# Optimization experiments

Hardware: AMD Instinct MI355X
Metric: run time of the kernel (lower is better)

Reference implementation:

```python
import jax, jax.numpy as jnp
import numpy as np

B, N, D, F, K = 32, 128, 3, 64, 50
EPS = 1e-6  # distances_from_vectors eps


def setup_inputs() -> dict:
    key = jax.random.key(0)
    ks = jax.random.split(key, 24)
    s = 0.1
    rn = lambda k, shape: (jax.random.normal(k, shape, jnp.float32) * s)
    return {
        "t": jnp.zeros((1,), jnp.float32),
        "xs": jax.random.normal(ks[0], (B, N * D), jnp.float32),
        "mus": jnp.linspace(0.0, 5.0, K).astype(jnp.float32),
        "gamma": jnp.array([10.0], jnp.float32),
        "W_enc": rn(ks[1], (1, F)), "b_enc": rn(ks[2], (F,)),
        "cf1_W1": rn(ks[3], (K, F)), "cf1_b1": rn(ks[4], (F,)),
        "cf1_W2": rn(ks[5], (F, F)), "cf1_b2": rn(ks[6], (F,)),
        "cf2_W1": rn(ks[7], (K, F)), "cf2_b1": rn(ks[8], (F,)),
        "cf2_W2": rn(ks[9], (F, F)), "cf2_b2": rn(ks[10], (F,)),
        "cf3_W1": rn(ks[11], (K, F)), "cf3_b1": rn(ks[12], (F,)),
        "cf3_W2": rn(ks[13], (F, F)), "cf3_b2": rn(ks[14], (F,)),
        "Wt1": rn(ks[15], (F, F)), "bt1": rn(ks[16], (F,)),
        "Wt2": rn(ks[17], (F, 1)), "bt2": rn(ks[18], (1,)),
    }


def reference(t, xs, mus, gamma, W_enc, b_enc,
              cf1_W1, cf1_b1, cf1_W2, cf1_b2,
              cf2_W1, cf2_b1, cf2_W2, cf2_b2,
              cf3_W1, cf3_b1, cf3_W2, cf3_b2,
              Wt1, bt1, Wt2, bt2):
    # off-diagonal neighbor index: row i -> all j != i  (N, N-1)
    idx = (jnp.arange(N)[:, None] + jnp.arange(1, N)[None, :]) % N

    def cfconv(rbf, W1, b1, W2, b2):
        return jax.nn.softplus(rbf @ W1 + b1) @ W2 + b2  # (B,N,N-1,F)

    def energy(xs_flat):
        x = xs_flat.reshape(B, N, D)
        nbr = x[:, idx, :]                       # (B,N,N-1,D)
        r = x[:, :, None, :] - nbr               # distance vectors
        d = jnp.sqrt(jnp.sum(r * r, -1) + EPS)[..., None]  # (B,N,N-1,1)
        rbf = jnp.exp(-gamma[0] * (d - mus) ** 2)          # (B,N,N-1,K)
        # feature_encoding(ones): Linear(1->F) of constant 1
        h = jnp.broadcast_to(W_enc[0] + b_enc, (B, N, F))
        for (W1, b1, W2, b2) in ((cf1_W1, cf1_b1, cf1_W2, cf1_b2),
                                 (cf2_W1, cf2_b1, cf2_W2, cf2_b2),
                                 (cf3_W1, cf3_b1, cf3_W2, cf3_b2)):
            # features[:, :, None, :] * W summed over neighbors == features * W.sum(2)
            Wsum = cfconv(rbf, W1, b1, W2, b2).sum(axis=2)  # (B,N,F)
            h = h + h * Wsum
        v = jnp.tanh(h @ Wt1 + bt1) @ Wt2 + bt2  # (B,N,1)
        return v.sum()

    dxs = -jax.grad(energy)(xs)                  # force = -dE/dx, (B, N*D)
    dxs = dxs.reshape(B, N, D)
    dxs = dxs - dxs.mean(axis=1, keepdims=True)  # remove mean over particles
    return dxs.reshape(B, N * D)
```

## Files before the change

### kernel.cpp

```cpp
#include <hip/hip_runtime.h>
#include <math.h>

#define NN 128
#define FF 64
#define KK 50
#define NI 640
#define EPSV 1e-6f


__device__ __forceinline__ float softplus_fast(float z) {
    float e = __expf(-fabsf(z));
    float l = __logf(1.f + e);
    return fmaxf(z, 0.f) + l;
}

__global__ __launch_bounds__(256) void k_dt(
    const float* __restrict__ xs, float* __restrict__ dws,
    const float* __restrict__ W1a, const float* __restrict__ W1b, const float* __restrict__ W1c,
    const float* __restrict__ b1a, const float* __restrict__ b1b, const float* __restrict__ b1c,
    const float* __restrict__ mus, const float* __restrict__ gamma,
    float4* __restrict__ Af, float4* __restrict__ Bf,
    const float* __restrict__ Wt1,
    const float* __restrict__ W2a, const float* __restrict__ W2b, const float* __restrict__ W2c,
    float* __restrict__ WT)
{
    int bid = blockIdx.x;
    if (bid < 2048) {
        int tid = bid * 256 + threadIdx.x;
        int b = tid >> 14;
        int rem = tid & 16383;
        int i = rem >> 7, a = rem & 127;
        const float* xb = xs + b * (NN * 3);
        float dx = xb[i*3+0] - xb[a*3+0];
        float dy = xb[i*3+1] - xb[a*3+1];
        float dz = xb[i*3+2] - xb[a*3+2];
        dws[tid] = sqrtf(dx*dx + dy*dy + dz*dz + EPSV);
        return;
    }
    if (bid < 2528) {
        int idx = (bid - 2048) * 256 + threadIdx.x;
        if (idx >= NI * 64 * 3) return;
        int l = idx / (NI * 64);
        int r = idx - l * (NI * 64);
        int j = r >> 6, f = r & 63;
        int base4 = j * 192 + f * 3;
        float h = 10.0f / (float)NI;
        float gam = gamma[0];
        const float* W  = (l == 0) ? W1a : (l == 1) ? W1b : W1c;
        const float* bb = (l == 0) ? b1a : (l == 1) ? b1b : b1c;
        float G[2], Gp[2], Gpp[2];
        float g2 = 4.f * gam * gam;
        for (int e = 0; e < 2; ++e) {
            float d = (float)(j + e) * h;
            float z = bb[f], zp = 0.f, zpp = 0.f;
            for (int k = 0; k < KK; ++k) {
                float x = d - mus[k];
                float ee = __expf(-gam * x * x);
                float we = W[k * 64 + f] * ee;
                z   += we;
                zp   = fmaf(we, -2.f * gam * x, zp);
                zpp  = fmaf(we, fmaf(g2 * x, x, -2.f * gam), zpp);
            }
            float sg = 1.f / (1.f + __expf(-z));
            G[e]   = softplus_fast(z);
            Gp[e]  = sg * zp;
            Gpp[e] = sg * (1.f - sg) * zp * zp + sg * zpp;
        }
        {
            float p0 = G[0], m0 = h * Gp[0], p1 = G[1], m1 = h * Gp[1];
            Af[base4 + l] = make_float4(
                p0, m0,
                3.f * (p1 - p0) - 2.f * m0 - m1,
                2.f * (p0 - p1) + m0 + m1);
        }
        {
            float q0 = Gp[0], n0 = h * Gpp[0], q1 = Gp[1], n1 = h * Gpp[1];
            Bf[base4 + l] = make_float4(
                q0, n0,
                3.f * (q1 - q0) - 2.f * n0 - n1,
                2.f * (q0 - q1) + n0 + n1);
        }
        return;
    }
    int idx = (bid - 2528) * 256 + threadIdx.x;
    if (idx < 16384) {
        int which = idx >> 12;
        int r = idx & 4095;
        int m = r >> 6, f = r & 63;
        const float* src = (which == 0) ? Wt1 : (which == 1) ? W2a : (which == 2) ? W2b : W2c;
        WT[idx] = src[f * 64 + m];
    }
}

__global__ __launch_bounds__(256) void k_fwdp(
    const float* __restrict__ dws, const float4* __restrict__ A4,
    float* __restrict__ usout)
{
    __shared__ float dsh[4][128];
    int tid = threadIdx.x;
    int wave = tid >> 6, lane = tid & 63;
    int atom = blockIdx.x * 4 + wave;
    int i = atom & 127;
    const float* drow = dws + (atom << 7);
    dsh[wave][lane]      = drow[lane];
    dsh[wave][64 + lane] = drow[64 + lane];
    const float invh = (float)NI / 10.0f;
    const float4* Afp = A4 + 3 * lane;
    double us0 = 0.0, us1 = 0.0, us2 = 0.0;

    #pragma unroll 1
    for (int g = 0; g < 4; ++g) {
        float ut0 = 0.f, ut1 = 0.f, ut2 = 0.f;
        int base = g << 5;
        int nb = (g == 3) ? 28 : 32;
        #pragma unroll 1
        for (int bb = 0; bb < nb; bb += 4) {
            float tt[4];
            float4 u0[4], u1[4], u2[4];
            #pragma unroll
            for (int p = 0; p < 4; ++p) {
                float d = dsh[wave][(i + 1 + base + bb + p) & 127];
                float fd = fminf(d * invh, (float)NI - 0.001f);
                float jf = floorf(fd);
                tt[p] = fd - jf;
                int j4 = (int)jf * 192;
                u0[p] = Afp[j4];
                u1[p] = Afp[j4 + 1];
                u2[p] = Afp[j4 + 2];
            }
            #pragma unroll
            for (int p = 0; p < 4; ++p) {
                float t1 = tt[p];
                ut0 += fmaf(t1, fmaf(t1, fmaf(t1, u0[p].w, u0[p].z), u0[p].y), u0[p].x);
                ut1 += fmaf(t1, fmaf(t1, fmaf(t1, u1[p].w, u1[p].z), u1[p].y), u1[p].x);
                ut2 += fmaf(t1, fmaf(t1, fmaf(t1, u2[p].w, u2[p].z), u2[p].y), u2[p].x);
            }
        }
        if (g == 3) {
            #pragma unroll
            for (int p = 124; p < 127; ++p) {
                float d = dsh[wave][(i + 1 + p) & 127];
                float fd = fminf(d * invh, (float)NI - 0.001f);
                float jf = floorf(fd);
                float t1 = fd - jf;
                int j4 = (int)jf * 192;
                float4 c0 = Afp[j4];
                float4 c1 = Afp[j4 + 1];
                float4 c2 = Afp[j4 + 2];
                ut0 += fmaf(t1, fmaf(t1, fmaf(t1, c0.w, c0.z), c0.y), c0.x);
                ut1 += fmaf(t1, fmaf(t1, fmaf(t1, c1.w, c1.z), c1.y), c1.x);
                ut2 += fmaf(t1, fmaf(t1, fmaf(t1, c2.w, c2.z), c2.y), c2.x);
            }
        }
        us0 += (double)ut0; us1 += (double)ut1; us2 += (double)ut2;
    }

    float* uo = usout + atom * 192;
    uo[lane]       = (float)us0;
    uo[64 + lane]  = (float)us1;
    uo[128 + lane] = (float)us2;
}

__global__ __launch_bounds__(256) void k_epi(
    float* __restrict__ CU,
    const float* __restrict__ W2a, const float* __restrict__ W2b, const float* __restrict__ W2c,
    const float* __restrict__ b2a, const float* __restrict__ b2b, const float* __restrict__ b2c,
    const float* __restrict__ Wenc, const float* __restrict__ benc,
    const float* __restrict__ Wt1, const float* __restrict__ bt1, const float* __restrict__ Wt2,
    const float* __restrict__ WT)
{
    __shared__ double epid[4][FF];
    __shared__ float  epif[4][FF];
    const float* Wt1T = WT;
    const float* W2aT = WT + 4096;
    const float* W2bT = WT + 8192;
    const float* W2cT = WT + 12288;
    int tid = threadIdx.x;
    int wave = tid >> 6, lane = tid & 63, f = lane;
    int atom = blockIdx.x * 4 + wave;

    double us0 = (double)CU[atom * 192 + lane];
    double us1 = (double)CU[atom * 192 + 64 + lane];
    double us2 = (double)CU[atom * 192 + 128 + lane];

    double wf0, wf1, wf2;
    {
        epid[wave][lane] = us0;
        double acc = 0.0;
        for (int m = 0; m < 64; ++m) acc += epid[wave][m] * (double)W2a[m*64 + f];
        wf0 = 1.0 + acc + 127.0 * (double)b2a[f];

        epid[wave][lane] = us1;
        double acc1 = 0.0;
        for (int m = 0; m < 64; ++m) acc1 += epid[wave][m] * (double)W2b[m*64 + f];
        wf1 = 1.0 + acc1 + 127.0 * (double)b2b[f];

        epid[wave][lane] = us2;
        double acc2 = 0.0;
        for (int m = 0; m < 64; ++m) acc2 += epid[wave][m] * (double)W2c[m*64 + f];
        wf2 = 1.0 + acc2 + 127.0 * (double)b2c[f];
    }
    double h0 = (double)Wenc[f] + (double)benc[f];
    double h  = h0 * wf0 * wf1 * wf2;
    epid[wave][lane] = h;
    double pre = (double)bt1[lane];
    for (int m = 0; m < 64; ++m) pre += epid[wave][m] * (double)Wt1[m*64 + lane];
    double tv = tanh(pre);
    float gv = (float)((1.0 - tv * tv) * (double)Wt2[lane]);

    float p1 = (float)(h0 * wf1 * wf2);
    float p2 = (float)(h0 * wf0 * wf2);
    float p3 = (float)(h0 * wf0 * wf1);

    epif[wave][lane] = gv;
    float dv = 0.f;
    for (int m = 0; m < 64; ++m) dv = fmaf(epif[wave][m], Wt1T[m*64 + lane], dv);

    float* co = CU + atom * 192;
    epif[wave][lane] = dv * p1;
    float c0 = 0.f;
    for (int m = 0; m < 64; ++m) c0 = fmaf(epif[wave][m], W2aT[m*64 + lane], c0);
    co[lane] = c0;

    epif[wave][lane] = dv * p2;
    float c1 = 0.f;
    for (int m = 0; m < 64; ++m) c1 = fmaf(epif[wave][m], W2bT[m*64 + lane], c1);
    co[64 + lane] = c1;

    epif[wave][lane] = dv * p3;
    float c2 = 0.f;
    for (int m = 0; m < 64; ++m) c2 = fmaf(epif[wave][m], W2cT[m*64 + lane], c2);
    co[128 + lane] = c2;
}

__global__ __launch_bounds__(256) void k_bwd(
    const float* __restrict__ dws, const float4* __restrict__ B4,
    const float* __restrict__ C, float* __restrict__ T)
{
    __shared__ float dsh[4][128];
    int tid = threadIdx.x;
    int wave = tid >> 6, lane = tid & 63;
    int atom = blockIdx.x * 4 + wave;
    int b = atom >> 7, i = atom & 127;
    const float* drow = dws + (atom << 7);
    dsh[wave][lane]      = drow[lane];
    dsh[wave][64 + lane] = drow[64 + lane];
    const float* ci = C + atom * 192;
    float ci0 = ci[lane], ci1 = ci[64 + lane], ci2 = ci[128 + lane];
    float* Tb = T + ((size_t)b << 14);
    const float invh = (float)NI / 10.0f;
    const float4* Bfp = B4 + 3 * lane;
    float vm = 0.f;

    #pragma unroll 1
    for (int g = 0; g < 16; ++g) {
        int offb = 1 + (g << 2);
        float tt[4], cA[4], cB[4], cC[4];
        float4 u0[4], u1[4], u2[4];
        #pragma unroll
        for (int p = 0; p < 4; ++p) {
            int aa = (i + offb + p) & 127;
            float d = dsh[wave][aa];
            float fd = fminf(d * invh, (float)NI - 0.001f);
            float jf = floorf(fd);
            tt[p] = fd - jf;
            int j4 = (int)jf * 192;
            u0[p] = Bfp[j4];
            u1[p] = Bfp[j4 + 1];
            u2[p] = Bfp[j4 + 2];
            const float* ca = C + (((b << 7) + aa) * 192);
            cA[p] = ca[lane]; cB[p] = ca[64 + lane]; cC[p] = ca[128 + lane];
        }
        #pragma unroll
        for (int p = 0; p < 4; ++p) {
            float t1 = tt[p];
            float g0 = fmaf(t1, fmaf(t1, fmaf(t1, u0[p].w, u0[p].z), u0[p].y), u0[p].x);
            float g1 = fmaf(t1, fmaf(t1, fmaf(t1, u1[p].w, u1[p].z), u1[p].y), u1[p].x);
            float g2 = fmaf(t1, fmaf(t1, fmaf(t1, u2[p].w, u2[p].z), u2[p].y), u2[p].x);
            float red = (ci0 + cA[p]) * g0 + (ci1 + cB[p]) * g1 + (ci2 + cC[p]) * g2;
            #pragma unroll
            for (int o = 1; o < 64; o <<= 1) red += __shfl_xor(red, o);
            if (lane == (g << 2) + p) vm = red;
        }
    }
    int off = lane + 1;
    if (off < 64 || i < 64) {
        int a = (i + off) & 127;
        Tb[(i << 7) + a] = vm;
        Tb[(a << 7) + i] = vm;
    }
}

__global__ __launch_bounds__(256) void k_force(
    const float* __restrict__ xs, const float* __restrict__ dws,
    const float* __restrict__ T, float* __restrict__ Fr)
{
    int tid = threadIdx.x;
    int wave = tid >> 6, lane = tid & 63;
    int atom = blockIdx.x * 4 + wave;
    int i = atom & 127;
    int b = atom >> 7;
    const float* xb = xs + b * (NN * 3);
    float xi0 = xb[i*3], xi1 = xb[i*3+1], xi2 = xb[i*3+2];
    const float* drow = dws + (atom << 7);
    const float* trow = T + (atom << 7);
    float fx = 0.f, fy = 0.f, fz = 0.f;
    for (int it = lane; it < 127; it += 64) {
        int aa = (i + 1 + it) & 127;
        float coef = trow[aa] / drow[aa];
        fx += coef * (xi0 - xb[aa*3]);
        fy += coef * (xi1 - xb[aa*3+1]);
        fz += coef * (xi2 - xb[aa*3+2]);
    }
    #pragma unroll
    for (int off = 1; off < 64; off <<= 1) {
        fx += __shfl_xor(fx, off);
        fy += __shfl_xor(fy, off);
        fz += __shfl_xor(fz, off);
    }
    if (lane == 0) {
        Fr[atom*3]   = fx;
        Fr[atom*3+1] = fy;
        Fr[atom*3+2] = fz;
    }
}

__global__ __launch_bounds__(128) void k_out(const float* __restrict__ Fr, float* __restrict__ out)
{
    __shared__ float rs[3][128];
    int b = blockIdx.x, n = threadIdx.x;
    float g0 = Fr[(b*128+n)*3], g1 = Fr[(b*128+n)*3+1], g2 = Fr[(b*128+n)*3+2];
    rs[0][n] = g0; rs[1][n] = g1; rs[2][n] = g2;
    __syncthreads();
    for (int s = 64; s > 0; s >>= 1) {
        if (n < s) {
            rs[0][n] += rs[0][n+s];
            rs[1][n] += rs[1][n+s];
            rs[2][n] += rs[2][n+s];
        }
        __syncthreads();
    }
    float m0 = rs[0][0] * (1.f/128.f);
    float m1 = rs[1][0] * (1.f/128.f);
    float m2 = rs[2][0] * (1.f/128.f);
    out[b*384 + n*3 + 0] = m0 - g0;
    out[b*384 + n*3 + 1] = m1 - g1;
    out[b*384 + n*3 + 2] = m2 - g2;
}

extern "C" void kernel_launch(void* const* d_in, const int* in_sizes, int n_in,
                              void* d_out, int out_size, void* d_ws, size_t ws_size,
                              hipStream_t stream)
{
    const float* xs   = (const float*)d_in[1];
    const float* mus  = (const float*)d_in[2];
    const float* gam  = (const float*)d_in[3];
    const float* Wenc = (const float*)d_in[4];
    const float* benc = (const float*)d_in[5];
    const float* W1a  = (const float*)d_in[6];
    const float* b1a  = (const float*)d_in[7];
    const float* W2a  = (const float*)d_in[8];
    const float* b2a  = (const float*)d_in[9];
    const float* W1b  = (const float*)d_in[10];
    const float* b1b  = (const float*)d_in[11];
    const float* W2b  = (const float*)d_in[12];
    const float* b2b  = (const float*)d_in[13];
    const float* W1c  = (const float*)d_in[14];
    const float* b1c  = (const float*)d_in[15];
    const float* W2c  = (const float*)d_in[16];
    const float* b2c  = (const float*)d_in[17];
    const float* Wt1  = (const float*)d_in[18];
    const float* bt1  = (const float*)d_in[19];
    const float* Wt2  = (const float*)d_in[20];

    float* ws  = (float*)d_ws;
    float* dws = ws;
    float* T   = ws + 524288;
    float4* A4 = (float4*)(ws + 1048576);
    float4* B4 = (float4*)(ws + 1540096);
    float* WT  = ws + 2031616;
    float* C   = ws + 2097152;
    float* Fr  = ws + 2883584;
    float* out = (float*)d_out;

    k_dt   <<<2592, 256, 0, stream>>>(xs, dws, W1a, W1b, W1c, b1a, b1b, b1c,
                                      mus, gam, A4, B4, Wt1, W2a, W2b, W2c, WT);
    k_fwdp <<<1024, 256, 0, stream>>>(dws, A4, C);
    k_epi  <<<1024, 256, 0, stream>>>(C, W2a, W2b, W2c, b2a, b2b, b2c,
                                      Wenc, benc, Wt1, bt1, Wt2, WT);
    k_bwd  <<<1024, 256, 0, stream>>>(dws, B4, C, T);
    k_force<<<1024, 256, 0, stream>>>(xs, dws, T, Fr);
    k_out  <<<32, 128, 0, stream>>>(Fr, out);
}
```

Baseline: 149.3 us.

## Split each atom's neighbor loop across two waves in forward and backward kernels

The forward-pass and backward-pass kernels now give each atom two wavefronts, each covering half of the neighbor range, instead of one wavefront per atom. Partial sums in the forward kernel are combined through shared memory, and in the backward kernel each wave writes its own 32 pair entries. Grid sizes double to keep atom coverage the same. This targets latency-bound per-atom serial loops by exposing more parallelism, at the cost of extra block syncs, LDS use, and a different accumulation order.

```diff
diff --git a/kernel.cpp b/kernel.cpp
--- a/kernel.cpp
+++ b/kernel.cpp
@@ -96,30 +96,36 @@
     const float* __restrict__ dws, const float4* __restrict__ A4,
     float* __restrict__ usout)
 {
-    __shared__ float dsh[4][128];
+    __shared__ float dsh[2][128];
+    __shared__ float ush[2][2][3][64];
     int tid = threadIdx.x;
     int wave = tid >> 6, lane = tid & 63;
-    int atom = blockIdx.x * 4 + wave;
+    int ai = wave >> 1, half = wave & 1;
+    int atom = blockIdx.x * 2 + ai;
     int i = atom & 127;
     const float* drow = dws + (atom << 7);
-    dsh[wave][lane]      = drow[lane];
-    dsh[wave][64 + lane] = drow[64 + lane];
+    dsh[ai][half * 64 + lane] = drow[half * 64 + lane];
+    __syncthreads();
+
     const float invh = (float)NI / 10.0f;
     const float4* Afp = A4 + 3 * lane;
     double us0 = 0.0, us1 = 0.0, us2 = 0.0;
+    int obase = 1 + (half << 6);
+    int lim = half ? 63 : 64;
 
     #pragma unroll 1
-    for (int g = 0; g < 4; ++g) {
+    for (int g = 0; g < 2; ++g) {
         float ut0 = 0.f, ut1 = 0.f, ut2 = 0.f;
-        int base = g << 5;
-        int nb = (g == 3) ? 28 : 32;
+        int gb = g << 5;
+        int nb = lim - gb; if (nb > 32) nb = 32;
+        int nb4 = nb & ~3;
         #pragma unroll 1
-        for (int bb = 0; bb < nb; bb += 4) {
+        for (int bb = 0; bb < nb4; bb += 4) {
             float tt[4];
             float4 u0[4], u1[4], u2[4];
             #pragma unroll
             for (int p = 0; p < 4; ++p) {
-                float d = dsh[wave][(i + 1 + base + bb + p) & 127];
+                float d = dsh[ai][(i + obase + gb + bb + p) & 127];
                 float fd = fminf(d * invh, (float)NI - 0.001f);
                 float jf = floorf(fd);
                 tt[p] = fd - jf;
@@ -136,29 +142,32 @@
                 ut2 += fmaf(t1, fmaf(t1, fmaf(t1, u2[p].w, u2[p].z), u2[p].y), u2[p].x);
             }
         }
-        if (g == 3) {
-            #pragma unroll
-            for (int p = 124; p < 127; ++p) {
-                float d = dsh[wave][(i + 1 + p) & 127];
-                float fd = fminf(d * invh, (float)NI - 0.001f);
-                float jf = floorf(fd);
-                float t1 = fd - jf;
-                int j4 = (int)jf * 192;
-                float4 c0 = Afp[j4];
-                float4 c1 = Afp[j4 + 1];
-                float4 c2 = Afp[j4 + 2];
-                ut0 += fmaf(t1, fmaf(t1, fmaf(t1, c0.w, c0.z), c0.y), c0.x);
-                ut1 += fmaf(t1, fmaf(t1, fmaf(t1, c1.w, c1.z), c1.y), c1.x);
-                ut2 += fmaf(t1, fmaf(t1, fmaf(t1, c2.w, c2.z), c2.y), c2.x);
-            }
+        for (int p = nb4; p < nb; ++p) {
+            float d = dsh[ai][(i + obase + gb + p) & 127];
+            float fd = fminf(d * invh, (float)NI - 0.001f);
+            float jf = floorf(fd);
+            float t1 = fd - jf;
+            int j4 = (int)jf * 192;
+            float4 c0 = Afp[j4];
+            float4 c1 = Afp[j4 + 1];
+            float4 c2 = Afp[j4 + 2];
+            ut0 += fmaf(t1, fmaf(t1, fmaf(t1, c0.w, c0.z), c0.y), c0.x);
+            ut1 += fmaf(t1, fmaf(t1, fmaf(t1, c1.w, c1.z), c1.y), c1.x);
+            ut2 += fmaf(t1, fmaf(t1, fmaf(t1, c2.w, c2.z), c2.y), c2.x);
         }
         us0 += (double)ut0; us1 += (double)ut1; us2 += (double)ut2;
     }
 
-    float* uo = usout + atom * 192;
-    uo[lane]       = (float)us0;
-    uo[64 + lane]  = (float)us1;
-    uo[128 + lane] = (float)us2;
+    ush[ai][half][0][lane] = (float)us0;
+    ush[ai][half][1][lane] = (float)us1;
+    ush[ai][half][2][lane] = (float)us2;
+    __syncthreads();
+    if (half == 0) {
+        float* uo = usout + atom * 192;
+        uo[lane]       = ush[ai][0][0][lane] + ush[ai][1][0][lane];
+        uo[64 + lane]  = ush[ai][0][1][lane] + ush[ai][1][1][lane];
+        uo[128 + lane] = ush[ai][0][2][lane] + ush[ai][1][2][lane];
+    }
 }
 
 __global__ __launch_bounds__(256) void k_epi(
@@ -237,14 +246,16 @@
     const float* __restrict__ dws, const float4* __restrict__ B4,
     const float* __restrict__ C, float* __restrict__ T)
 {
-    __shared__ float dsh[4][128];
+    __shared__ float dsh[2][128];
     int tid = threadIdx.x;
     int wave = tid >> 6, lane = tid & 63;
-    int atom = blockIdx.x * 4 + wave;
+    int ai = wave >> 1, half = wave & 1;
+    int atom = blockIdx.x * 2 + ai;
     int b = atom >> 7, i = atom & 127;
     const float* drow = dws + (atom << 7);
-    dsh[wave][lane]      = drow[lane];
-    dsh[wave][64 + lane] = drow[64 + lane];
+    dsh[ai][half * 64 + lane] = drow[half * 64 + lane];
+    __syncthreads();
+
     const float* ci = C + atom * 192;
     float ci0 = ci[lane], ci1 = ci[64 + lane], ci2 = ci[128 + lane];
     float* Tb = T + ((size_t)b << 14);
@@ -253,14 +264,14 @@
     float vm = 0.f;
 
     #pragma unroll 1
-    for (int g = 0; g < 16; ++g) {
-        int offb = 1 + (g << 2);
+    for (int g = 0; g < 8; ++g) {
+        int offb = 1 + (half << 5) + (g << 2);
         float tt[4], cA[4], cB[4], cC[4];
         float4 u0[4], u1[4], u2[4];
         #pragma unroll
         for (int p = 0; p < 4; ++p) {
             int aa = (i + offb + p) & 127;
-            float d = dsh[wave][aa];
+            float d = dsh[ai][aa];
             float fd = fminf(d * invh, (float)NI - 0.001f);
             float jf = floorf(fd);
             tt[p] = fd - jf;
@@ -283,8 +294,8 @@
             if (lane == (g << 2) + p) vm = red;
         }
     }
-    int off = lane + 1;
-    if (off < 64 || i < 64) {
+    int off = 1 + (half << 5) + lane;
+    if (lane < 32 && (off < 64 || i < 64)) {
         int a = (i + off) & 127;
         Tb[(i << 7) + a] = vm;
         Tb[(a << 7) + i] = vm;
@@ -385,10 +396,10 @@
 
     k_dt   <<<2592, 256, 0, stream>>>(xs, dws, W1a, W1b, W1c, b1a, b1b, b1c,
                                       mus, gam, A4, B4, Wt1, W2a, W2b, W2c, WT);
-    k_fwdp <<<1024, 256, 0, stream>>>(dws, A4, C);
+    k_fwdp <<<2048, 256, 0, stream>>>(dws, A4, C);
     k_epi  <<<1024, 256, 0, stream>>>(C, W2a, W2b, W2c, b2a, b2b, b2c,
                                       Wenc, benc, Wt1, bt1, Wt2, WT);
-    k_bwd  <<<1024, 256, 0, stream>>>(dws, B4, C, T);
+    k_bwd  <<<2048, 256, 0, stream>>>(dws, B4, C, T);
     k_force<<<1024, 256, 0, stream>>>(xs, dws, T, Fr);
     k_out  <<<32, 128, 0, stream>>>(Fr, out);
 }
```

Measured after the change: 157.0 us. 1.05x slower.
